# Performance work log

Measured on AMD Instinct MI355X. Metric: run time of the kernel, lower is better.

The kernel has to match this reference:

```python
import jax, jax.numpy as jnp
import numpy as np

DEGREE_RES = 15
NUM_ROT = int(np.ceil(360 / DEGREE_RES))  # 24
PIXEL_SIZE = 0.0625
IM_METERS = 4.0
IM_SIZE = int(IM_METERS / PIXEL_SIZE)  # 64


def _create_rot_mat():
    angles = np.radians([i * DEGREE_RES for i in range(NUM_ROT)])
    c, s = np.cos(angles), np.sin(angles)
    rot = np.stack([
        np.stack([c, np.zeros_like(c), -s], axis=-1),
        np.stack([np.zeros_like(c), np.ones_like(c), np.zeros_like(c)], axis=-1),
        np.stack([s, np.zeros_like(c), c], axis=-1),
    ], axis=1)  # [NUM_ROT, 3, 3]
    return jnp.asarray(rot, dtype=jnp.float32)


def setup_inputs() -> dict:
    key = jax.random.key(0)
    xyz = jax.random.normal(key, (32, 16384, 3), dtype=jnp.float32)
    rot_mat = _create_rot_mat()
    return {"xyz": xyz, "rot_mat": rot_mat}


def reference(xyz, rot_mat):
    B, N, _ = xyz.shape
    R = rot_mat.shape[0]
    # rotate each point by each rotation: [B, R, N, 3]
    xyz_rot = jnp.einsum('rij,bnj->brni', rot_mat, xyz)
    # project x,z -> pixel indices (offset by half image extent, 2 meters)
    proj = jnp.round((xyz_rot[..., :2] + IM_METERS / 2) / PIXEL_SIZE).astype(jnp.int32)
    mask = ((proj[..., 0] >= 0) & (proj[..., 0] < IM_SIZE) &
            (proj[..., 1] >= 0) & (proj[..., 1] < IM_SIZE))
    # out-of-range points are zeroed -> they (faithfully) write at pixel (0,0)
    proj = proj * mask[..., None]
    vals = xyz_rot[..., 2] / 10.0  # non-occupancy branch: scatter z/10
    image = jnp.zeros((B, R, IM_SIZE, IM_SIZE), dtype=xyz.dtype)
    b = jnp.arange(B)[:, None, None]
    r = jnp.arange(R)[None, :, None]
    image = image.at[b, r, proj[..., 1], proj[..., 0]].set(vals)
    return image
```

## Files before the change

kernel.cpp:

```cpp
#include <hip/hip_runtime.h>
#include <stdint.h>

#define BB 32
#define NN 16384
#define RR 24
#define IMS 64
#define NPIX (IMS * IMS)
#define RPB 3
#define GROUPS (RR / RPB)
#define SCRATCH (RPB * 64)
#define LDSN (RPB * NPIX + SCRATCH)

__global__ __launch_bounds__(1024) void rotproj_lds(
    const float* __restrict__ xyz, const float* __restrict__ rot,
    float* __restrict__ out) {
  __shared__ unsigned int img[LDSN];

  const int blk = blockIdx.x;
  const int b = blk >> 3;
  const int rg = blk & (GROUPS - 1);

  for (int i = threadIdx.x; i < LDSN; i += 1024) img[i] = 0u;

  const float* m = rot + rg * RPB * 9;
  float c0[RPB], c2[RPB], c6[RPB], c8[RPB];
#pragma unroll
  for (int rl = 0; rl < RPB; ++rl) {
    c0[rl] = m[rl * 9 + 0];
    c2[rl] = m[rl * 9 + 2];
    c6[rl] = m[rl * 9 + 6];
    c8[rl] = m[rl * 9 + 8];
  }

  const int w = threadIdx.x >> 6;
  const int lane = threadIdx.x & 63;
  int srel[RPB];
#pragma unroll
  for (int rl = 0; rl < RPB; ++rl)
    srel[rl] = (RPB - rl) * NPIX + rl * 64 + lane;

  __syncthreads();

  const float* pts = xyz + (size_t)b * NN * 3;

#pragma unroll
  for (int iter = 0; iter < 2; ++iter) {
    const int nbase = w * 1024 + iter * 512 + lane;
    float X[8], Y[8], Z[8];
#pragma unroll
    for (int jj = 0; jj < 8; ++jj) {
      const float* p = pts + 3 * (nbase + jj * 64);
      X[jj] = p[0];
      Y[jj] = p[1];
      Z[jj] = p[2];
    }

#pragma unroll
    for (int jj = 0; jj < 8; ++jj) {
      const float x = X[jj], y = Y[jj], z = Z[jj];
      const int n = nbase + jj * 64;

      const int py = (int)rintf(__fmaf_rn(y, 16.0f, 32.0f));
      const bool pyin = (unsigned)py < (unsigned)IMS;
      const int pybase = py * IMS;
      const int s = 37 * py;
      const unsigned int nkey = (unsigned)(n + 1) << 17;

#pragma unroll
      for (int rl = 0; rl < RPB; ++rl) {
        const float xr =
            __fadd_rn(__fmul_rn(c0[rl], x), __fmul_rn(c2[rl], z));
        const float zr = __fmaf_rn(c6[rl], x, __fmul_rn(c8[rl], z));

        const int px = (int)rintf(__fmaf_rn(xr, 16.0f, 32.0f));
        const bool in = ((unsigned)px < (unsigned)IMS) & pyin;

        const unsigned int key = nkey | (__float_as_uint(zr) >> 15);

        const int slot = pybase + ((px + s) & 63);
        const int word = in ? slot : srel[rl];
        (void)__hip_atomic_fetch_max(&img[rl * NPIX + word], key,
                                     __ATOMIC_RELAXED,
                                     __HIP_MEMORY_SCOPE_WORKGROUP);
      }
    }
  }

  __syncthreads();

  if (threadIdx.x < SCRATCH) {
    const unsigned int k = img[RPB * NPIX + threadIdx.x];
    if (k)
      (void)__hip_atomic_fetch_max(&img[(threadIdx.x >> 6) * NPIX], k,
                                   __ATOMIC_RELAXED,
                                   __HIP_MEMORY_SCOPE_WORKGROUP);
  }

  __syncthreads();

  float* oslice = out + ((size_t)b * RR + (size_t)rg * RPB) * NPIX;
#pragma unroll
  for (int t = 0; t < RPB * NPIX / 4096; ++t) {
    const int i = (t * 1024 + threadIdx.x) * 4;
    const int py = (i >> 6) & (IMS - 1);
    const int rowbase = i & ~(IMS - 1);
    const int s = 37 * py;
    float4 o;
    float* po = &o.x;
#pragma unroll
    for (int q = 0; q < 4; ++q) {
      const int px = (i + q) & (IMS - 1);
      const unsigned int k = img[rowbase | ((px + s) & (IMS - 1))];
      const float zr = __uint_as_float((k & 0x1FFFFu) << 15);
      po[q] = k ? (zr / 10.0f) : 0.0f;
    }
    *(float4*)(&oslice[i]) = o;
  }
}

extern "C" void kernel_launch(void* const* d_in, const int* in_sizes, int n_in,
                              void* d_out, int out_size, void* d_ws,
                              size_t ws_size, hipStream_t stream) {
  const float* xyz = (const float*)d_in[0];
  const float* rot = (const float*)d_in[1];
  float* out = (float*)d_out;

  rotproj_lds<<<BB * GROUPS, 1024, 0, stream>>>(xyz, rot, out);
}
```

Before: 70.21 us.

## Assign one rotation per block instead of three per block

Each block now handles a single (batch, rotation) pair, so the grid grows from 256 to 768 blocks, each using one 64x64 LDS image. The goal is more parallelism and occupancy across CUs and a smaller per-block LDS footprint. The cost is that every block re-reads the same batch's point cloud from global memory, which triples point-load traffic, and the per-block setup and zeroing overhead is repeated more often.

```diff
diff --git a/kernel.cpp b/kernel.cpp
--- a/kernel.cpp
+++ b/kernel.cpp
@@ -6,38 +6,27 @@
 #define RR 24
 #define IMS 64
 #define NPIX (IMS * IMS)
-#define RPB 3
-#define GROUPS (RR / RPB)
-#define SCRATCH (RPB * 64)
-#define LDSN (RPB * NPIX + SCRATCH)
+#define LDSN (NPIX + 64)
 
-__global__ __launch_bounds__(1024) void rotproj_lds(
+__global__ __launch_bounds__(1024, 8) void rotproj_lds(
     const float* __restrict__ xyz, const float* __restrict__ rot,
     float* __restrict__ out) {
   __shared__ unsigned int img[LDSN];
 
   const int blk = blockIdx.x;
-  const int b = blk >> 3;
-  const int rg = blk & (GROUPS - 1);
+  const int b = blk / RR;
+  const int r = blk - b * RR;
 
   for (int i = threadIdx.x; i < LDSN; i += 1024) img[i] = 0u;
 
-  const float* m = rot + rg * RPB * 9;
-  float c0[RPB], c2[RPB], c6[RPB], c8[RPB];
-#pragma unroll
-  for (int rl = 0; rl < RPB; ++rl) {
-    c0[rl] = m[rl * 9 + 0];
-    c2[rl] = m[rl * 9 + 2];
-    c6[rl] = m[rl * 9 + 6];
-    c8[rl] = m[rl * 9 + 8];
-  }
+  const float c0 = rot[r * 9 + 0];
+  const float c2 = rot[r * 9 + 2];
+  const float c6 = rot[r * 9 + 6];
+  const float c8 = rot[r * 9 + 8];
 
   const int w = threadIdx.x >> 6;
   const int lane = threadIdx.x & 63;
-  int srel[RPB];
-#pragma unroll
-  for (int rl = 0; rl < RPB; ++rl)
-    srel[rl] = (RPB - rl) * NPIX + rl * 64 + lane;
+  const int scr = NPIX + lane;
 
   __syncthreads();
 
@@ -62,60 +51,49 @@
 
       const int py = (int)rintf(__fmaf_rn(y, 16.0f, 32.0f));
       const bool pyin = (unsigned)py < (unsigned)IMS;
-      const int pybase = py * IMS;
-      const int s = 37 * py;
-      const unsigned int nkey = (unsigned)(n + 1) << 17;
 
-#pragma unroll
-      for (int rl = 0; rl < RPB; ++rl) {
-        const float xr =
-            __fadd_rn(__fmul_rn(c0[rl], x), __fmul_rn(c2[rl], z));
-        const float zr = __fmaf_rn(c6[rl], x, __fmul_rn(c8[rl], z));
+      const float xr = __fadd_rn(__fmul_rn(c0, x), __fmul_rn(c2, z));
+      const float zr = __fmaf_rn(c6, x, __fmul_rn(c8, z));
 
-        const int px = (int)rintf(__fmaf_rn(xr, 16.0f, 32.0f));
-        const bool in = ((unsigned)px < (unsigned)IMS) & pyin;
+      const int px = (int)rintf(__fmaf_rn(xr, 16.0f, 32.0f));
+      const bool in = ((unsigned)px < (unsigned)IMS) & pyin;
 
-        const unsigned int key = nkey | (__float_as_uint(zr) >> 15);
+      const unsigned int key =
+          ((unsigned)(n + 1) << 17) | (__float_as_uint(zr) >> 15);
 
-        const int slot = pybase + ((px + s) & 63);
-        const int word = in ? slot : srel[rl];
-        (void)__hip_atomic_fetch_max(&img[rl * NPIX + word], key,
-                                     __ATOMIC_RELAXED,
-                                     __HIP_MEMORY_SCOPE_WORKGROUP);
-      }
+      const int slot = py * IMS + ((px + 37 * py) & 63);
+      const int word = in ? slot : scr;
+      (void)__hip_atomic_fetch_max(&img[word], key, __ATOMIC_RELAXED,
+                                   __HIP_MEMORY_SCOPE_WORKGROUP);
     }
   }
 
   __syncthreads();
 
-  if (threadIdx.x < SCRATCH) {
-    const unsigned int k = img[RPB * NPIX + threadIdx.x];
+  if (threadIdx.x < 64) {
+    const unsigned int k = img[NPIX + threadIdx.x];
     if (k)
-      (void)__hip_atomic_fetch_max(&img[(threadIdx.x >> 6) * NPIX], k,
-                                   __ATOMIC_RELAXED,
+      (void)__hip_atomic_fetch_max(&img[0], k, __ATOMIC_RELAXED,
                                    __HIP_MEMORY_SCOPE_WORKGROUP);
   }
 
   __syncthreads();
 
-  float* oslice = out + ((size_t)b * RR + (size_t)rg * RPB) * NPIX;
+  float* oslice = out + ((size_t)b * RR + r) * NPIX;
+  const int i = threadIdx.x * 4;
+  const int py = i >> 6;
+  const int rowbase = i & ~(IMS - 1);
+  const int s = 37 * py;
+  float4 o;
+  float* po = &o.x;
 #pragma unroll
-  for (int t = 0; t < RPB * NPIX / 4096; ++t) {
-    const int i = (t * 1024 + threadIdx.x) * 4;
-    const int py = (i >> 6) & (IMS - 1);
-    const int rowbase = i & ~(IMS - 1);
-    const int s = 37 * py;
-    float4 o;
-    float* po = &o.x;
-#pragma unroll
-    for (int q = 0; q < 4; ++q) {
-      const int px = (i + q) & (IMS - 1);
-      const unsigned int k = img[rowbase | ((px + s) & (IMS - 1))];
-      const float zr = __uint_as_float((k & 0x1FFFFu) << 15);
-      po[q] = k ? (zr / 10.0f) : 0.0f;
-    }
-    *(float4*)(&oslice[i]) = o;
+  for (int q = 0; q < 4; ++q) {
+    const int px = (i + q) & (IMS - 1);
+    const unsigned int k = img[rowbase | ((px + s) & (IMS - 1))];
+    const float zr = __uint_as_float((k & 0x1FFFFu) << 15);
+    po[q] = k ? (zr / 10.0f) : 0.0f;
   }
+  *(float4*)(&oslice[i]) = o;
 }
 
 extern "C" void kernel_launch(void* const* d_in, const int* in_sizes, int n_in,
@@ -125,5 +103,5 @@
   const float* rot = (const float*)d_in[1];
   float* out = (float*)d_out;
 
-  rotproj_lds<<<BB * GROUPS, 1024, 0, stream>>>(xyz, rot, out);
+  rotproj_lds<<<BB * RR, 1024, 0, stream>>>(xyz, rot, out);
 }
```

After: 75.41 us. +7.4%, slower.
